# Kernel tuning notes

Measured on AMD Instinct MI355X. Metric: run time of the kernel, lower is better.

Reference implementation:

```python
import jax, jax.numpy as jnp
import numpy as np

B, C, L = 4, 256, 4096
C8 = C // 8

def setup_inputs() -> dict:
    key = jax.random.key(0)
    ks = jax.random.split(key, 8)
    s = 1.0 / np.sqrt(C)
    x = jax.random.normal(ks[0], (B, C, L), dtype=jnp.float32)
    Wq = jax.random.normal(ks[1], (C8, C), dtype=jnp.float32) * s
    bq = jax.random.normal(ks[2], (C8,), dtype=jnp.float32) * s
    Wk = jax.random.normal(ks[3], (C8, C), dtype=jnp.float32) * s
    bk = jax.random.normal(ks[4], (C8,), dtype=jnp.float32) * s
    Wv = jax.random.normal(ks[5], (C, C), dtype=jnp.float32) * s
    bv = jax.random.normal(ks[6], (C,), dtype=jnp.float32) * s
    gamma = jax.random.normal(ks[7], (1,), dtype=jnp.float32) * 0.1
    return {"x": x, "Wq": Wq, "bq": bq, "Wk": Wk, "bk": bk, "Wv": Wv, "bv": bv, "gamma": gamma}

def reference(x, Wq, bq, Wk, bk, Wv, bv, gamma):
    # pointwise conv1d == channel matmul: [O,C] x [B,C,L] -> [B,O,L]
    q = jnp.einsum('oc,bcl->bol', Wq, x) + bq[None, :, None]   # [B, C8, L]
    k = jnp.einsum('oc,bcl->bol', Wk, x) + bk[None, :, None]   # [B, C8, L]
    v = jnp.einsum('oc,bcl->bol', Wv, x) + bv[None, :, None]   # [B, C,  L]
    # attention[b,i,j] = sum_c q[b,c,i] * k[b,c,j]
    attn = jnp.einsum('bci,bcj->bij', q, k)                    # [B, L, L]
    attn = jax.nn.softmax(attn, axis=-1)
    # out[b,c,i] = sum_j v[b,c,j] * attn[b,i,j]
    out = jnp.einsum('bcj,bij->bci', v, attn)                  # [B, C, L]
    return gamma * out + x
```

## Files before the change

kernel.cpp:

```cpp
#include <hip/hip_runtime.h>
#include <math.h>

#define BB 4
#define CC 256
#define LL 4096
#define DD 32
#define LOG2E 1.44269504088896f

typedef __attribute__((ext_vector_type(8))) short short8;
typedef __attribute__((ext_vector_type(4))) short short4v;
typedef __attribute__((ext_vector_type(4))) float f32x4;
typedef __attribute__((ext_vector_type(4))) unsigned int uint4v;
typedef __attribute__((ext_vector_type(2))) unsigned int uint2v;

#define BARRIER() asm volatile("s_waitcnt lgkmcnt(0)\n\ts_barrier" ::: "memory")

__device__ inline unsigned short f2bf(float f) {
  union { float f; unsigned u; } v; v.f = f;
  unsigned r = v.u + 0x7fffu + ((v.u >> 16) & 1u);
  return (unsigned short)(r >> 16);
}

__device__ inline float fast_exp2(float x) {
#if __has_builtin(__builtin_amdgcn_exp2f)
  return __builtin_amdgcn_exp2f(x);
#else
  return exp2f(x);
#endif
}

__device__ __host__ inline int sigma32(int p) {
  const int q4 = (p >> 3) & 3, u = p & 7;
  return 16 * (u >> 2) + 4 * q4 + (u & 3);
}

__global__ __launch_bounds__(256) void wprep_kernel(
    const float* __restrict__ Wq, const float* __restrict__ Wk, const float* __restrict__ Wv,
    unsigned short* __restrict__ wf)
{
  const int t = threadIdx.x;
  const int ot = blockIdx.x >> 1;
  const int rep = blockIdx.x & 1;
  const int lane = t & 63, cl = lane & 15, q4 = lane >> 4;
  const int ks = (t >> 6) + 4 * rep;
  const int o = ot * 16 + cl;
  const int c = ks * 32 + q4 * 8;
  const float* src = (o < 32) ? (Wq + o * CC) : (o < 64) ? (Wk + (o - 32) * CC)
                                              : (Wv + (o - 64) * CC);
  const float sc = (o < 32) ? LOG2E : 1.0f;
  unsigned short p[8];
  #pragma unroll
  for (int j = 0; j < 8; ++j) p[j] = f2bf(src[c + j] * sc);
  uint4v u;
  u.x = (unsigned)p[0] | ((unsigned)p[1] << 16);
  u.y = (unsigned)p[2] | ((unsigned)p[3] << 16);
  u.z = (unsigned)p[4] | ((unsigned)p[5] << 16);
  u.w = (unsigned)p[6] | ((unsigned)p[7] << 16);
  *(uint4v*)(wf + ((size_t)(ot * 8 + ks) * 64 + lane) * 8) = u;
}

__global__ __launch_bounds__(512, 4) void qkv_kernel(
    const float* __restrict__ x, const unsigned short* __restrict__ wf,
    const float* __restrict__ bq, const float* __restrict__ bk, const float* __restrict__ bv,
    unsigned short* __restrict__ qT, unsigned short* __restrict__ kT,
    unsigned short* __restrict__ vf)
{
  __shared__ union {
    float xl[32 * 261];
    struct {
      unsigned short qk[32 * 72];
      __align__(16) unsigned short v[256 * 40];
    } ep;
  } sm;

  const int t = threadIdx.x;
  const int lane = t & 63, cl = lane & 15, q4 = lane >> 4;
  const int blk = blockIdx.x;
  const int b  = (blk & 7) >> 1;
  const int it = ((blk >> 3) << 1) + (blk & 1);
  const int i0 = it * 32;

  {
    const int ln8 = t & 7;
    #pragma unroll
    for (int p = 0; p < 4; ++p) {
      const int c = (t >> 3) + 64 * p;
      const f32x4 v = *(const f32x4*)(x + ((size_t)(b * CC + c)) * LL + i0 + ln8 * 4);
      #pragma unroll
      for (int k = 0; k < 4; ++k) sm.xl[(ln8 * 4 + k) * 261 + c] = v[k];
    }
  }
  __syncthreads();

  const int wi = (t >> 6) & 1, wo = t >> 7;
  const f32x4 zero = {0.f, 0.f, 0.f, 0.f};
  f32x4 acc[5];
  #pragma unroll
  for (int u = 0; u < 5; ++u) acc[u] = zero;

  for (int ks = 0; ks < 8; ++ks) {
    unsigned short p[8];
    #pragma unroll
    for (int j = 0; j < 8; ++j)
      p[j] = f2bf(sm.xl[(16 * wi + cl) * 261 + ks * 32 + q4 * 8 + j]);
    union { short8 s; uint4v u; } bfr;
    bfr.u.x = (unsigned)p[0] | ((unsigned)p[1] << 16);
    bfr.u.y = (unsigned)p[2] | ((unsigned)p[3] << 16);
    bfr.u.z = (unsigned)p[4] | ((unsigned)p[5] << 16);
    bfr.u.w = (unsigned)p[6] | ((unsigned)p[7] << 16);
    #pragma unroll
    for (int u = 0; u < 5; ++u) {
      const short8 a = *(const short8*)(wf + ((size_t)((wo * 5 + u) * 8 + ks) * 64 + lane) * 8);
      acc[u] = __builtin_amdgcn_mfma_f32_16x16x32_bf16(a, bfr.s, acc[u], 0, 0, 0);
    }
  }
  __syncthreads();

  #pragma unroll
  for (int u = 0; u < 5; ++u) {
    const int g = wo * 5 + u;
    if (g < 4) {
      short4v pk;
      #pragma unroll
      for (int r = 0; r < 4; ++r) {
        const int o = 16 * g + 4 * q4 + r;
        const float v = acc[u][r] + ((o < 32) ? bq[o] * LOG2E : bk[o - 32]);
        pk[r] = (short)f2bf(v);
      }
      *(short4v*)&sm.ep.qk[(16 * wi + cl) * 72 + 16 * g + 4 * q4] = pk;
    } else {
      #pragma unroll
      for (int r = 0; r < 4; ++r) {
        const int ch = 16 * (g - 4) + 4 * q4 + r;
        sm.ep.v[ch * 40 + 16 * wi + cl] = f2bf(acc[u][r] + bv[ch]);
      }
    }
  }
  __syncthreads();

  if (t < 64) {
    const int i = t >> 1, which = t & 1;
    const int gi = i0 + i;
    const unsigned short* srcp = &sm.ep.qk[i * 72 + which * 32];
    uint4v d0 = *(const uint4v*)(srcp + 0);
    uint4v d1 = *(const uint4v*)(srcp + 8);
    uint4v d2 = *(const uint4v*)(srcp + 16);
    uint4v d3 = *(const uint4v*)(srcp + 24);
    unsigned short* dst;
    if (which == 0) {
      dst = qT + ((size_t)b * LL + gi) * DD;
    } else {
      const int row = (gi & ~31) + sigma32(gi & 31);
      dst = kT + ((size_t)b * LL + row) * DD;
    }
    *(uint4v*)dst = d0; *(uint4v*)(dst + 8) = d1;
    *(uint4v*)(dst + 16) = d2; *(uint4v*)(dst + 24) = d3;
  }
  const int kk = it & 1, jt = it >> 1;
  #pragma unroll
  for (int rep = 0; rep < 2; ++rep) {
    const int slot = t + 512 * rep;
    const int fl = slot >> 6, l2 = slot & 63;
    const int cl2 = l2 & 15, q42 = l2 >> 4;
    const int m4 = fl >> 2, mt = fl & 3;
    const int fg = 8 * m4 + 4 * kk + mt;
    const int ch = 64 * m4 + 16 * mt + cl2;
    const uint4v d = *(const uint4v*)&sm.ep.v[ch * 40 + q42 * 8];
    *(uint4v*)(vf + (((size_t)(b * 64 + jt)) * 32 + fg) * 512 + l2 * 8) = d;
  }
}

__global__ __launch_bounds__(1024, 4) void attn_kernel(
    const unsigned short* __restrict__ qT, const unsigned short* __restrict__ kT,
    const unsigned short* __restrict__ vf, const float* __restrict__ x,
    const float* __restrict__ gamma_p, float* __restrict__ out)
{
  __shared__ union __align__(16) {
    unsigned short P[2][8][4][2][64][4];
    float OmA[2][4][16][64][4];
  } sm;
  __shared__ float l_lds[16][4][64];
  __shared__ float l2[4][4][64];
  __shared__ __align__(16) unsigned short qls[4 * 64 * 8];

  const int t = threadIdx.x;
  const int w = t >> 6, lane = t & 63, cl = lane & 15, q4 = lane >> 4;
  const int kk_a = w & 7, ha = w >> 3;
  const int m4 = w & 3, kp = w >> 2;
  const int blk = blockIdx.x;
  const int b  = (blk & 7) >> 1;
  const int it = ((blk >> 3) << 1) + (blk & 1);
  const int i0 = it * 64;

  if (t < 256) {
    const int nt = t >> 6, lq = t & 63, clq = lq & 15, q4q = lq >> 4;
    *(uint4v*)&qls[t * 8] =
        *(const uint4v*)(qT + ((size_t)b * LL + i0 + 16 * nt + clq) * DD + q4q * 8);
  }

  const f32x4 zero = {0.f, 0.f, 0.f, 0.f};
  f32x4 O[4][4];
  #pragma unroll
  for (int mt = 0; mt < 4; ++mt)
    #pragma unroll
    for (int nt = 0; nt < 4; ++nt) O[mt][nt] = zero;
  float l_r[4] = {0.f, 0.f, 0.f, 0.f};

  const unsigned short* kbase =
      kT + ((size_t)b * LL + 32 * kk_a + 16 * ha + cl) * DD + q4 * 8;
  const unsigned short* vroot = vf + ((size_t)(b * 64)) * 32 * 512 + lane * 8;

  short8 kb = *(const short8*)kbase;
  short8 va[4];
  {
    const int g = 2 * kp;
    const size_t base = ((size_t)(g >> 1) * 32 + 8 * m4 + 4 * (g & 1)) * 512;
    #pragma unroll
    for (int mt = 0; mt < 4; ++mt)
      va[mt] = *(const short8*)(vroot + base + mt * 512);
  }
  __syncthreads();

  for (int ss = 0; ss < 16; ++ss) {
    const int buf = ss & 1;

    f32x4 s[4];
    __builtin_amdgcn_s_setprio(1);
    #pragma unroll
    for (int nt = 0; nt < 4; ++nt)
      s[nt] = __builtin_amdgcn_mfma_f32_16x16x32_bf16(
          kb, *(const short8*)&qls[(nt * 64 + lane) * 8], zero, 0, 0, 0);
    __builtin_amdgcn_s_setprio(0);
    kb = *(const short8*)(kbase + (size_t)(((ss + 1) & 15) * 256) * DD);

    #pragma unroll
    for (int nt = 0; nt < 4; ++nt) {
      const float e0 = fast_exp2(s[nt][0]);
      const float e1 = fast_exp2(s[nt][1]);
      const float e2 = fast_exp2(s[nt][2]);
      const float e3 = fast_exp2(s[nt][3]);
      uint2v uv;
      uv.x = __builtin_amdgcn_perm(__float_as_uint(e1), __float_as_uint(e0), 0x07060302);
      uv.y = __builtin_amdgcn_perm(__float_as_uint(e3), __float_as_uint(e2), 0x07060302);
      *(uint2v*)&sm.P[buf][kk_a][nt][ha][lane][0] = uv;
      l_r[nt] += (e0 + e1) + (e2 + e3);
    }
    BARRIER();

    #pragma unroll
    for (int e = 0; e < 2; ++e) {
      const int kk = 2 * kp + e;
      short8 pb[4];
      #pragma unroll
      for (int nt = 0; nt < 4; ++nt) {
        union { short8 s8; uint2v h[2]; } pbu;
        pbu.h[0] = *(const uint2v*)&sm.P[buf][kk][nt][0][lane][0];
        pbu.h[1] = *(const uint2v*)&sm.P[buf][kk][nt][1][lane][0];
        pb[nt] = pbu.s8;
      }
      __builtin_amdgcn_s_setprio(1);
      #pragma unroll
      for (int mt = 0; mt < 4; ++mt)
        #pragma unroll
        for (int nt = 0; nt < 4; ++nt)
          O[mt][nt] = __builtin_amdgcn_mfma_f32_16x16x32_bf16(va[mt], pb[nt],
                                                              O[mt][nt], 0, 0, 0);
      __builtin_amdgcn_s_setprio(0);
      const int nss = e ? ((ss + 1) & 15) : ss;
      const int g = nss * 8 + 2 * kp + (e ^ 1);
      const size_t base = ((size_t)(g >> 1) * 32 + 8 * m4 + 4 * (g & 1)) * 512;
      #pragma unroll
      for (int mt = 0; mt < 4; ++mt)
        va[mt] = *(const short8*)(vroot + base + mt * 512);
    }
  }

  #pragma unroll
  for (int nt = 0; nt < 4; ++nt)
    l_lds[w][nt][lane] = l_r[nt];
  BARRIER();

  {
    const int ntp = w >> 2, part = w & 3;
    float sl = l_lds[part * 4 + 0][ntp][lane] + l_lds[part * 4 + 1][ntp][lane]
             + l_lds[part * 4 + 2][ntp][lane] + l_lds[part * 4 + 3][ntp][lane];
    l2[part][ntp][lane] = sl;
  }
  if (kp >= 2) {
    #pragma unroll
    for (int mt = 0; mt < 4; ++mt)
      #pragma unroll
      for (int nt = 0; nt < 4; ++nt)
        *(f32x4*)&sm.OmA[kp - 2][m4][mt * 4 + nt][lane][0] = O[mt][nt];
  }
  BARRIER();
  if (kp < 2) {
    #pragma unroll
    for (int mt = 0; mt < 4; ++mt)
      #pragma unroll
      for (int nt = 0; nt < 4; ++nt)
        O[mt][nt] += *(const f32x4*)&sm.OmA[kp][m4][mt * 4 + nt][lane][0];
  }
  BARRIER();
  if (kp == 1) {
    #pragma unroll
    for (int mt = 0; mt < 4; ++mt)
      #pragma unroll
      for (int nt = 0; nt < 4; ++nt)
        *(f32x4*)&sm.OmA[0][m4][mt * 4 + nt][lane][0] = O[mt][nt];
  }
  BARRIER();
  if (kp == 0) {
    const float gam = gamma_p[0];
    float inv_l[4];
    #pragma unroll
    for (int nt = 0; nt < 4; ++nt) {
      float s = 0.f;
      #pragma unroll
      for (int part = 0; part < 4; ++part)
        #pragma unroll
        for (int g = 0; g < 4; ++g)
          s += l2[part][nt][g * 16 + cl];
      inv_l[nt] = 1.0f / s;
    }
    #pragma unroll
    for (int mt = 0; mt < 4; ++mt) {
      #pragma unroll
      for (int nt = 0; nt < 4; ++nt) {
        const f32x4 om = *(const f32x4*)&sm.OmA[0][m4][mt * 4 + nt][lane][0];
        #pragma unroll
        for (int r = 0; r < 4; ++r) {
          const int ch = 64 * m4 + 16 * mt + 4 * q4 + r;
          const int i  = i0 + 16 * nt + cl;
          const size_t idx = ((size_t)b * CC + ch) * LL + i;
          out[idx] = gam * (O[mt][nt][r] + om[r]) * inv_l[nt] + x[idx];
        }
      }
    }
  }
}

extern "C" void kernel_launch(void* const* d_in, const int* in_sizes, int n_in,
                              void* d_out, int out_size, void* d_ws, size_t ws_size,
                              hipStream_t stream) {
  const float* x     = (const float*)d_in[0];
  const float* Wq    = (const float*)d_in[1];
  const float* bq    = (const float*)d_in[2];
  const float* Wk    = (const float*)d_in[3];
  const float* bk    = (const float*)d_in[4];
  const float* Wv    = (const float*)d_in[5];
  const float* bv    = (const float*)d_in[6];
  const float* gamma = (const float*)d_in[7];
  float* out = (float*)d_out;

  unsigned short* qT = (unsigned short*)d_ws;
  unsigned short* kT = qT + (size_t)BB * LL * DD;
  unsigned short* vf = kT + (size_t)BB * LL * DD;
  unsigned short* wf = (unsigned short*)d_out;

  wprep_kernel<<<40, 256, 0, stream>>>(Wq, Wk, Wv, wf);
  qkv_kernel<<<512, 512, 0, stream>>>(x, wf, bq, bk, bv, qT, kT, vf);
  attn_kernel<<<256, 1024, 0, stream>>>(qT, kT, vf, x, gamma, out);
}
```

Before: 136.1 us.

## Process two key sub-tiles per barrier with quad-buffered P and double-buffered V

Unrolls the attention loop by two so each iteration computes scores and exp for two key sub-tiles into four P buffers before one barrier, then runs four PV MFMA phases. This halves the number of workgroup barriers and gives more independent work between synchronisations. It doubles the K and V register prefetch buffers and the P shared-memory footprint, which raises register and LDS pressure under a 1024-thread launch bound.

New measurement: 195.8 us. 43.9% more time.

```diff
diff --git a/kernel.cpp b/kernel.cpp
--- a/kernel.cpp
+++ b/kernel.cpp
@@ -176,7 +176,7 @@
     const float* __restrict__ gamma_p, float* __restrict__ out)
 {
   __shared__ union __align__(16) {
-    unsigned short P[2][8][4][2][64][4];
+    unsigned short P[4][8][4][2][64][4];
     float OmA[2][4][16][64][4];
   } sm;
   __shared__ float l_lds[16][4][64];
@@ -210,52 +210,78 @@
       kT + ((size_t)b * LL + 32 * kk_a + 16 * ha + cl) * DD + q4 * 8;
   const unsigned short* vroot = vf + ((size_t)(b * 64)) * 32 * 512 + lane * 8;
 
-  short8 kb = *(const short8*)kbase;
-  short8 va[4];
-  {
-    const int g = 2 * kp;
+  short8 kb[2];
+  kb[0] = *(const short8*)kbase;
+  kb[1] = *(const short8*)(kbase + (size_t)256 * DD);
+
+  short8 va[2][4];
+  #pragma unroll
+  for (int e = 0; e < 2; ++e) {
+    const int g = 2 * kp + e;
     const size_t base = ((size_t)(g >> 1) * 32 + 8 * m4 + 4 * (g & 1)) * 512;
     #pragma unroll
     for (int mt = 0; mt < 4; ++mt)
-      va[mt] = *(const short8*)(vroot + base + mt * 512);
+      va[e][mt] = *(const short8*)(vroot + base + mt * 512);
   }
   __syncthreads();
 
-  for (int ss = 0; ss < 16; ++ss) {
-    const int buf = ss & 1;
-
-    f32x4 s[4];
+  for (int it2 = 0; it2 < 8; ++it2) {
+    const int ss0 = 2 * it2;
+    const int b0 = ss0 & 3, b1 = b0 + 1;
+
+    f32x4 s0[4];
     __builtin_amdgcn_s_setprio(1);
     #pragma unroll
     for (int nt = 0; nt < 4; ++nt)
-      s[nt] = __builtin_amdgcn_mfma_f32_16x16x32_bf16(
-          kb, *(const short8*)&qls[(nt * 64 + lane) * 8], zero, 0, 0, 0);
+      s0[nt] = __builtin_amdgcn_mfma_f32_16x16x32_bf16(
+          kb[0], *(const short8*)&qls[(nt * 64 + lane) * 8], zero, 0, 0, 0);
     __builtin_amdgcn_s_setprio(0);
-    kb = *(const short8*)(kbase + (size_t)(((ss + 1) & 15) * 256) * DD);
-
+    kb[0] = *(const short8*)(kbase + (size_t)(((ss0 + 2) & 15) * 256) * DD);
     #pragma unroll
     for (int nt = 0; nt < 4; ++nt) {
-      const float e0 = fast_exp2(s[nt][0]);
-      const float e1 = fast_exp2(s[nt][1]);
-      const float e2 = fast_exp2(s[nt][2]);
-      const float e3 = fast_exp2(s[nt][3]);
+      const float e0 = fast_exp2(s0[nt][0]);
+      const float e1 = fast_exp2(s0[nt][1]);
+      const float e2 = fast_exp2(s0[nt][2]);
+      const float e3 = fast_exp2(s0[nt][3]);
       uint2v uv;
       uv.x = __builtin_amdgcn_perm(__float_as_uint(e1), __float_as_uint(e0), 0x07060302);
       uv.y = __builtin_amdgcn_perm(__float_as_uint(e3), __float_as_uint(e2), 0x07060302);
-      *(uint2v*)&sm.P[buf][kk_a][nt][ha][lane][0] = uv;
+      *(uint2v*)&sm.P[b0][kk_a][nt][ha][lane][0] = uv;
       l_r[nt] += (e0 + e1) + (e2 + e3);
     }
+
+    f32x4 s1[4];
+    __builtin_amdgcn_s_setprio(1);
+    #pragma unroll
+    for (int nt = 0; nt < 4; ++nt)
+      s1[nt] = __builtin_amdgcn_mfma_f32_16x16x32_bf16(
+          kb[1], *(const short8*)&qls[(nt * 64 + lane) * 8], zero, 0, 0, 0);
+    __builtin_amdgcn_s_setprio(0);
+    kb[1] = *(const short8*)(kbase + (size_t)(((ss0 + 3) & 15) * 256) * DD);
+    #pragma unroll
+    for (int nt = 0; nt < 4; ++nt) {
+      const float e0 = fast_exp2(s1[nt][0]);
+      const float e1 = fast_exp2(s1[nt][1]);
+      const float e2 = fast_exp2(s1[nt][2]);
+      const float e3 = fast_exp2(s1[nt][3]);
+      uint2v uv;
+      uv.x = __builtin_amdgcn_perm(__float_as_uint(e1), __float_as_uint(e0), 0x07060302);
+      uv.y = __builtin_amdgcn_perm(__float_as_uint(e3), __float_as_uint(e2), 0x07060302);
+      *(uint2v*)&sm.P[b1][kk_a][nt][ha][lane][0] = uv;
+      l_r[nt] += (e0 + e1) + (e2 + e3);
+    }
     BARRIER();
 
     #pragma unroll
-    for (int e = 0; e < 2; ++e) {
-      const int kk = 2 * kp + e;
+    for (int e = 0; e < 4; ++e) {
+      const int bufe = (e < 2) ? b0 : b1;
+      const int kk = 2 * kp + (e & 1);
       short8 pb[4];
       #pragma unroll
       for (int nt = 0; nt < 4; ++nt) {
         union { short8 s8; uint2v h[2]; } pbu;
-        pbu.h[0] = *(const uint2v*)&sm.P[buf][kk][nt][0][lane][0];
-        pbu.h[1] = *(const uint2v*)&sm.P[buf][kk][nt][1][lane][0];
+        pbu.h[0] = *(const uint2v*)&sm.P[bufe][kk][nt][0][lane][0];
+        pbu.h[1] = *(const uint2v*)&sm.P[bufe][kk][nt][1][lane][0];
         pb[nt] = pbu.s8;
       }
       __builtin_amdgcn_s_setprio(1);
@@ -263,15 +289,15 @@
       for (int mt = 0; mt < 4; ++mt)
         #pragma unroll
         for (int nt = 0; nt < 4; ++nt)
-          O[mt][nt] = __builtin_amdgcn_mfma_f32_16x16x32_bf16(va[mt], pb[nt],
+          O[mt][nt] = __builtin_amdgcn_mfma_f32_16x16x32_bf16(va[e & 1][mt], pb[nt],
                                                               O[mt][nt], 0, 0, 0);
       __builtin_amdgcn_s_setprio(0);
-      const int nss = e ? ((ss + 1) & 15) : ss;
-      const int g = nss * 8 + 2 * kp + (e ^ 1);
+      const int nss = (e < 2) ? (ss0 + 1) : ((ss0 + 2) & 15);
+      const int g = nss * 8 + 2 * kp + (e & 1);
       const size_t base = ((size_t)(g >> 1) * 32 + 8 * m4 + 4 * (g & 1)) * 512;
       #pragma unroll
       for (int mt = 0; mt < 4; ++mt)
-        va[mt] = *(const short8*)(vroot + base + mt * 512);
+        va[e & 1][mt] = *(const short8*)(vroot + base + mt * 512);
     }
   }
 
```

## Repartition PV work to 8 channel groups x 2 key halves with 2-step barriers

Applied to the files above, without the earlier changes.

The PV stage is split into 8 channel groups of 32 channels and 2 key halves, instead of 4 channel groups of 64 channels and 4 key quarters. This halves each wave's O accumulator registers and shrinks the cross-wave reduction to a single LDS exchange. The main loop now handles two score steps per barrier using a 4-deep P buffer, halving the number of barriers. The cost is a larger P buffer in LDS and more V-fragment loads per wave, since each V fragment now feeds fewer MFMAs.

After: 133.4 us. 1.02x faster.

```diff
diff --git a/kernel.cpp b/kernel.cpp
--- a/kernel.cpp
+++ b/kernel.cpp
@@ -176,17 +176,18 @@
     const float* __restrict__ gamma_p, float* __restrict__ out)
 {
   __shared__ union __align__(16) {
-    unsigned short P[2][8][4][2][64][4];
-    float OmA[2][4][16][64][4];
+    unsigned short P[4][8][4][2][64][4];
+    float Om[8][8][64][4];
   } sm;
   __shared__ float l_lds[16][4][64];
-  __shared__ float l2[4][4][64];
+  __shared__ float l2s[4][4][64];
   __shared__ __align__(16) unsigned short qls[4 * 64 * 8];
 
   const int t = threadIdx.x;
   const int w = t >> 6, lane = t & 63, cl = lane & 15, q4 = lane >> 4;
   const int kk_a = w & 7, ha = w >> 3;
-  const int m4 = w & 3, kp = w >> 2;
+  const int m8 = w & 7, kp = w >> 3;
+  const int m4 = m8 >> 1, mtA = 2 * (m8 & 1);
   const int blk = blockIdx.x;
   const int b  = (blk & 7) >> 1;
   const int it = ((blk >> 3) << 1) + (blk & 1);
@@ -199,57 +200,88 @@
   }
 
   const f32x4 zero = {0.f, 0.f, 0.f, 0.f};
-  f32x4 O[4][4];
-  #pragma unroll
-  for (int mt = 0; mt < 4; ++mt)
-    #pragma unroll
-    for (int nt = 0; nt < 4; ++nt) O[mt][nt] = zero;
+  f32x4 O[2][4];
+  #pragma unroll
+  for (int j = 0; j < 2; ++j)
+    #pragma unroll
+    for (int nt = 0; nt < 4; ++nt) O[j][nt] = zero;
   float l_r[4] = {0.f, 0.f, 0.f, 0.f};
 
   const unsigned short* kbase =
       kT + ((size_t)b * LL + 32 * kk_a + 16 * ha + cl) * DD + q4 * 8;
   const unsigned short* vroot = vf + ((size_t)(b * 64)) * 32 * 512 + lane * 8;
 
-  short8 kb = *(const short8*)kbase;
-  short8 va[4];
-  {
-    const int g = 2 * kp;
-    const size_t base = ((size_t)(g >> 1) * 32 + 8 * m4 + 4 * (g & 1)) * 512;
-    #pragma unroll
-    for (int mt = 0; mt < 4; ++mt)
-      va[mt] = *(const short8*)(vroot + base + mt * 512);
+  short8 kb[2];
+  kb[0] = *(const short8*)kbase;
+  kb[1] = *(const short8*)(kbase + (size_t)256 * DD);
+
+  short8 va[2][2];
+  #pragma unroll
+  for (int e = 0; e < 2; ++e) {
+    const int g = 4 * kp + e;
+    const size_t base = ((size_t)(g >> 1) * 32 + 8 * m4 + 4 * (g & 1) + mtA) * 512;
+    #pragma unroll
+    for (int j = 0; j < 2; ++j)
+      va[e][j] = *(const short8*)(vroot + base + j * 512);
   }
   __syncthreads();
 
-  for (int ss = 0; ss < 16; ++ss) {
-    const int buf = ss & 1;
-
-    f32x4 s[4];
-    __builtin_amdgcn_s_setprio(1);
-    #pragma unroll
-    for (int nt = 0; nt < 4; ++nt)
-      s[nt] = __builtin_amdgcn_mfma_f32_16x16x32_bf16(
-          kb, *(const short8*)&qls[(nt * 64 + lane) * 8], zero, 0, 0, 0);
-    __builtin_amdgcn_s_setprio(0);
-    kb = *(const short8*)(kbase + (size_t)(((ss + 1) & 15) * 256) * DD);
-
-    #pragma unroll
-    for (int nt = 0; nt < 4; ++nt) {
-      const float e0 = fast_exp2(s[nt][0]);
-      const float e1 = fast_exp2(s[nt][1]);
-      const float e2 = fast_exp2(s[nt][2]);
-      const float e3 = fast_exp2(s[nt][3]);
-      uint2v uv;
-      uv.x = __builtin_amdgcn_perm(__float_as_uint(e1), __float_as_uint(e0), 0x07060302);
-      uv.y = __builtin_amdgcn_perm(__float_as_uint(e3), __float_as_uint(e2), 0x07060302);
-      *(uint2v*)&sm.P[buf][kk_a][nt][ha][lane][0] = uv;
-      l_r[nt] += (e0 + e1) + (e2 + e3);
+  for (int it2 = 0; it2 < 8; ++it2) {
+    const int ss0 = 2 * it2;
+    const int b0 = ss0 & 3;
+
+    {
+      f32x4 s[4];
+      __builtin_amdgcn_s_setprio(1);
+      #pragma unroll
+      for (int nt = 0; nt < 4; ++nt)
+        s[nt] = __builtin_amdgcn_mfma_f32_16x16x32_bf16(
+            kb[0], *(const short8*)&qls[(nt * 64 + lane) * 8], zero, 0, 0, 0);
+      __builtin_amdgcn_s_setprio(0);
+      kb[0] = *(const short8*)(kbase + (size_t)(((ss0 + 2) & 15) * 256) * DD);
+      #pragma unroll
+      for (int nt = 0; nt < 4; ++nt) {
+        const float e0 = fast_exp2(s[nt][0]);
+        const float e1 = fast_exp2(s[nt][1]);
+        const float e2 = fast_exp2(s[nt][2]);
+        const float e3 = fast_exp2(s[nt][3]);
+        uint2v uv;
+        uv.x = __builtin_amdgcn_perm(__float_as_uint(e1), __float_as_uint(e0), 0x07060302);
+        uv.y = __builtin_amdgcn_perm(__float_as_uint(e3), __float_as_uint(e2), 0x07060302);
+        *(uint2v*)&sm.P[b0][kk_a][nt][ha][lane][0] = uv;
+        l_r[nt] += (e0 + e1) + (e2 + e3);
+      }
+    }
+
+    {
+      f32x4 s[4];
+      __builtin_amdgcn_s_setprio(1);
+      #pragma unroll
+      for (int nt = 0; nt < 4; ++nt)
+        s[nt] = __builtin_amdgcn_mfma_f32_16x16x32_bf16(
+            kb[1], *(const short8*)&qls[(nt * 64 + lane) * 8], zero, 0, 0, 0);
+      __builtin_amdgcn_s_setprio(0);
+      kb[1] = *(const short8*)(kbase + (size_t)(((ss0 + 3) & 15) * 256) * DD);
+      #pragma unroll
+      for (int nt = 0; nt < 4; ++nt) {
+        const float e0 = fast_exp2(s[nt][0]);
+        const float e1 = fast_exp2(s[nt][1]);
+        const float e2 = fast_exp2(s[nt][2]);
+        const float e3 = fast_exp2(s[nt][3]);
+        uint2v uv;
+        uv.x = __builtin_amdgcn_perm(__float_as_uint(e1), __float_as_uint(e0), 0x07060302);
+        uv.y = __builtin_amdgcn_perm(__float_as_uint(e3), __float_as_uint(e2), 0x07060302);
+        *(uint2v*)&sm.P[b0 + 1][kk_a][nt][ha][lane][0] = uv;
+        l_r[nt] += (e0 + e1) + (e2 + e3);
+      }
     }
     BARRIER();
 
     #pragma unroll
-    for (int e = 0; e < 2; ++e) {
-      const int kk = 2 * kp + e;
+    for (int ee = 0; ee < 8; ++ee) {
+      const int e = ee & 3;
+      const int kk = 4 * kp + e;
+      const int buf = b0 + (ee >> 2);
       short8 pb[4];
       #pragma unroll
       for (int nt = 0; nt < 4; ++nt) {
@@ -260,18 +292,19 @@
       }
       __builtin_amdgcn_s_setprio(1);
       #pragma unroll
-      for (int mt = 0; mt < 4; ++mt)
+      for (int j = 0; j < 2; ++j)
         #pragma unroll
         for (int nt = 0; nt < 4; ++nt)
-          O[mt][nt] = __builtin_amdgcn_mfma_f32_16x16x32_bf16(va[mt], pb[nt],
-                                                              O[mt][nt], 0, 0, 0);
+          O[j][nt] = __builtin_amdgcn_mfma_f32_16x16x32_bf16(va[ee & 1][j], pb[nt],
+                                                             O[j][nt], 0, 0, 0);
       __builtin_amdgcn_s_setprio(0);
-      const int nss = e ? ((ss + 1) & 15) : ss;
-      const int g = nss * 8 + 2 * kp + (e ^ 1);
-      const size_t base = ((size_t)(g >> 1) * 32 + 8 * m4 + 4 * (g & 1)) * 512;
-      #pragma unroll
-      for (int mt = 0; mt < 4; ++mt)
-        va[mt] = *(const short8*)(vroot + base + mt * 512);
+      const int nee = ee + 2;
+      const int nss = (ss0 + (nee >> 2)) & 15;
+      const int g = nss * 8 + 4 * kp + (nee & 3);
+      const size_t base = ((size_t)(g >> 1) * 32 + 8 * m4 + 4 * (g & 1) + mtA) * 512;
+      #pragma unroll
+      for (int j = 0; j < 2; ++j)
+        va[ee & 1][j] = *(const short8*)(vroot + base + j * 512);
     }
   }
 
@@ -284,30 +317,14 @@
     const int ntp = w >> 2, part = w & 3;
     float sl = l_lds[part * 4 + 0][ntp][lane] + l_lds[part * 4 + 1][ntp][lane]
              + l_lds[part * 4 + 2][ntp][lane] + l_lds[part * 4 + 3][ntp][lane];
-    l2[part][ntp][lane] = sl;
-  }
-  if (kp >= 2) {
-    #pragma unroll
-    for (int mt = 0; mt < 4; ++mt)
+    l2s[part][ntp][lane] = sl;
+  }
+  if (kp == 1) {
+    #pragma unroll
+    for (int j = 0; j < 2; ++j)
       #pragma unroll
       for (int nt = 0; nt < 4; ++nt)
-        *(f32x4*)&sm.OmA[kp - 2][m4][mt * 4 + nt][lane][0] = O[mt][nt];
-  }
-  BARRIER();
-  if (kp < 2) {
-    #pragma unroll
-    for (int mt = 0; mt < 4; ++mt)
-      #pragma unroll
-      for (int nt = 0; nt < 4; ++nt)
-        O[mt][nt] += *(const f32x4*)&sm.OmA[kp][m4][mt * 4 + nt][lane][0];
-  }
-  BARRIER();
-  if (kp == 1) {
-    #pragma unroll
-    for (int mt = 0; mt < 4; ++mt)
-      #pragma unroll
-      for (int nt = 0; nt < 4; ++nt)
-        *(f32x4*)&sm.OmA[0][m4][mt * 4 + nt][lane][0] = O[mt][nt];
+        *(f32x4*)&sm.Om[m8][j * 4 + nt][lane][0] = O[j][nt];
   }
   BARRIER();
   if (kp == 0) {
@@ -320,20 +337,20 @@
       for (int part = 0; part < 4; ++part)
         #pragma unroll
         for (int g = 0; g < 4; ++g)
-          s += l2[part][nt][g * 16 + cl];
+          s += l2s[part][nt][g * 16 + cl];
       inv_l[nt] = 1.0f / s;
     }
     #pragma unroll
-    for (int mt = 0; mt < 4; ++mt) {
+    for (int j = 0; j < 2; ++j) {
       #pragma unroll
       for (int nt = 0; nt < 4; ++nt) {
-        const f32x4 om = *(const f32x4*)&sm.OmA[0][m4][mt * 4 + nt][lane][0];
+        const f32x4 om = *(const f32x4*)&sm.Om[m8][j * 4 + nt][lane][0];
         #pragma unroll
         for (int r = 0; r < 4; ++r) {
-          const int ch = 64 * m4 + 16 * mt + 4 * q4 + r;
+          const int ch = 32 * m8 + 16 * j + 4 * q4 + r;
           const int i  = i0 + 16 * nt + cl;
           const size_t idx = ((size_t)b * CC + ch) * LL + i;
-          out[idx] = gam * (O[mt][nt][r] + om[r]) * inv_l[nt] + x[idx];
+          out[idx] = gam * (O[j][nt][r] + om[r]) * inv_l[nt] + x[idx];
         }
       }
     }
```
